# Performance work log

Measured on AMD Instinct MI355X. Metric: run time of the kernel, lower is better.

## Reference

```python
import jax, jax.numpy as jnp
import numpy as np

KS = 3  # kernel_size
PAD = 1  # padding


def setup_inputs() -> dict:
    key = jax.random.key(0)
    ks = jax.random.split(key, 5)
    b, c, h, w = 8, 64, 512, 512
    x = jax.random.normal(ks[0], (b, c, h, w), dtype=jnp.float32)
    w1 = jax.random.normal(ks[1], (c, c), dtype=jnp.float32) * 0.05
    b1 = jax.random.normal(ks[2], (c,), dtype=jnp.float32) * 0.05
    w2 = jax.random.normal(ks[3], (KS * KS, c), dtype=jnp.float32) * 0.05
    b2 = jax.random.normal(ks[4], (KS * KS,), dtype=jnp.float32) * 0.05
    return {"x": x, "w1": w1, "b1": b1, "w2": w2, "b2": b2}


def reference(x, w1, b1, w2, b2):
    b, c, h, w = x.shape
    # SEKG: global average pool -> 1x1 conv -> LeakyReLU(0.2) -> 1x1 conv
    feat = x.mean(axis=(2, 3))                      # [b, c]
    h1 = feat @ w1.T + b1                           # [b, c]
    h1 = jnp.where(h1 > 0, h1, 0.2 * h1)            # LeakyReLU(0.2)
    k = h1 @ w2.T + b2                              # [b, KS*KS]
    k = k.reshape(b, KS, KS)
    k = k / (k.sum(axis=(1, 2), keepdims=True) + 1e-6)  # normalize per-sample kernel
    # per-sample depthwise conv: fold batch into groups
    kern = jnp.broadcast_to(k[:, None], (b, c, KS, KS)).reshape(b * c, 1, KS, KS)
    xr = x.reshape(1, b * c, h, w)
    out = jax.lax.conv_general_dilated(
        xr, kern,
        window_strides=(1, 1),
        padding=[(PAD, PAD), (PAD, PAD)],
        feature_group_count=b * c,
        dimension_numbers=("NCHW", "OIHW", "NCHW"),
    )
    return out.reshape(b, c, h, w)
```

## Files before the change

kernel.cpp:

```cpp
#include <hip/hip_runtime.h>

#define HH 512
#define WW 512
#define HW (HH * WW)

typedef float f32x4 __attribute__((ext_vector_type(4)));

__device__ __forceinline__ void load_row6(float r[6], const float* __restrict__ plane,
                                          int y, int x0) {
    if ((unsigned)y >= (unsigned)HH) {
        r[0] = r[1] = r[2] = r[3] = r[4] = r[5] = 0.f;
        return;
    }
    const float* row = plane + (size_t)y * WW;
    r[0] = (x0 > 0) ? row[x0 - 1] : 0.f;
    const float4 m = *reinterpret_cast<const float4*>(row + x0);
    r[1] = m.x; r[2] = m.y; r[3] = m.z; r[4] = m.w;
    r[5] = (x0 + 4 < WW) ? row[x0 + 4] : 0.f;
}

__global__ __launch_bounds__(256) void stage_kernel(
        const float* __restrict__ x, float* __restrict__ out,
        float* __restrict__ partial,
        const float* __restrict__ w1, const float* __restrict__ b1,
        const float* __restrict__ w2, const float* __restrict__ b2,
        int ib, int nconv) {
    const int blk = blockIdx.x;
    const int t = threadIdx.x;

    if (blk < nconv) {
        const int b = ib - 1;
        __shared__ float feat[64];
        __shared__ float h1s[64];
        __shared__ float kks[10];
        if (t < 64) {
            const float* p4 = partial + (size_t)(b * 64 + t) * 4;
            feat[t] = (p4[0] + p4[1] + p4[2] + p4[3]) * (1.0f / (float)HW);
        }
        __syncthreads();
        if (t < 64) {
            float s = b1[t];
            const float* wr = w1 + t * 64;
            #pragma unroll 8
            for (int c = 0; c < 64; ++c) s += feat[c] * wr[c];
            h1s[t] = (s > 0.f) ? s : 0.2f * s;
        }
        __syncthreads();
        if (t < 9) {
            float s2 = b2[t];
            const float* wq = w2 + t * 64;
            #pragma unroll 8
            for (int c = 0; c < 64; ++c) s2 += h1s[c] * wq[c];
            kks[t] = s2;
        }
        __syncthreads();
        if (t == 0) {
            float s3 = 0.f;
            #pragma unroll
            for (int q = 0; q < 9; ++q) s3 += kks[q];
            kks[9] = s3 + 1e-6f;
        }
        __syncthreads();
        float k[9];
        {
            const float ks = kks[9];
            #pragma unroll
            for (int q = 0; q < 9; ++q) k[q] = kks[q] / ks;
        }

        const int plane_local = blk >> 4;
        const int plane = b * 64 + plane_local;
        const int xseg = t & 127;
        const int ystrip = ((blk & 15) << 1) | (t >> 7);
        const float* xp = x + (size_t)plane * HW;
        float* op       = out + (size_t)plane * HW;
        const int x0 = xseg * 4;
        const int y0 = ystrip * 16;

        float r0[6], r1[6], r2[6];
        load_row6(r0, xp, y0 - 1, x0);
        load_row6(r1, xp, y0,     x0);
        #pragma unroll
        for (int i = 0; i < 16; ++i) {
            load_row6(r2, xp, y0 + i + 1, x0);
            f32x4 o;
            #pragma unroll
            for (int j = 0; j < 4; ++j) {
                o[j] = k[0]*r0[j] + k[1]*r0[j+1] + k[2]*r0[j+2]
                     + k[3]*r1[j] + k[4]*r1[j+1] + k[5]*r1[j+2]
                     + k[6]*r2[j] + k[7]*r2[j+1] + k[8]*r2[j+2];
            }
            __builtin_nontemporal_store(o,
                reinterpret_cast<f32x4*>(op + (size_t)(y0 + i) * WW + x0));
            #pragma unroll
            for (int q = 0; q < 6; ++q) { r0[q] = r1[q]; r1[q] = r2[q]; }
        }
    } else {
        const int pblk = blk - nconv;
        const int plane = ib * 64 + (pblk >> 2);
        const int strip = pblk & 3;
        const float4* p = reinterpret_cast<const float4*>(x + (size_t)plane * HW) +
                          (size_t)strip * (HW / 16);
        float s = 0.f;
        #pragma unroll 4
        for (int i = t; i < HW / 16; i += 256) {
            float4 v = p[i];
            s += (v.x + v.y) + (v.z + v.w);
        }
        #pragma unroll
        for (int off = 32; off > 0; off >>= 1) s += __shfl_down(s, off, 64);
        __shared__ float wsum[4];
        const int lane = t & 63;
        const int wid  = t >> 6;
        if (lane == 0) wsum[wid] = s;
        __syncthreads();
        if (t == 0)
            partial[(size_t)plane * 4 + strip] =
                (wsum[0] + wsum[1]) + (wsum[2] + wsum[3]);
    }
}

extern "C" void kernel_launch(void* const* d_in, const int* in_sizes, int n_in,
                              void* d_out, int out_size, void* d_ws, size_t ws_size,
                              hipStream_t stream) {
    const float* x  = (const float*)d_in[0];
    const float* w1 = (const float*)d_in[1];
    const float* b1 = (const float*)d_in[2];
    const float* w2 = (const float*)d_in[3];
    const float* b2 = (const float*)d_in[4];
    float* out = (float*)d_out;
    float* partial = (float*)d_ws;

    stage_kernel<<<256, 256, 0, stream>>>(x, out, partial, w1, b1, w2, b2, 0, 0);
    for (int i = 1; i <= 7; ++i)
        stage_kernel<<<1280, 256, 0, stream>>>(x, out, partial, w1, b1, w2, b2, i, 1024);
    stage_kernel<<<1024, 256, 0, stream>>>(x, out, partial, w1, b1, w2, b2, 8, 1024);
}
```

Baseline: 302.2 us.

## Replace per-batch pipelined stages with a full pool pass and an XCD-mapped conv

The nine staggered launches, which overlapped pooling of batch i with convolution of batch i-1, are replaced by two kernels. One pass pools all planes, then a single conv grid runs over everything. Each conv block's batch is chosen from blockIdx & 7, so each XCD handles one batch's planes, which may improve L2 locality. In exchange the pool and conv phases no longer overlap, x is read twice without cache reuse between the stages, and every conv block recomputes the small MLP.

```diff
diff --git a/kernel.cpp b/kernel.cpp
--- a/kernel.cpp
+++ b/kernel.cpp
@@ -5,6 +5,29 @@
 #define HW (HH * WW)
 
 typedef float f32x4 __attribute__((ext_vector_type(4)));
+
+__global__ __launch_bounds__(256) void pool_kernel(const float* __restrict__ x,
+                                                   float* __restrict__ partial) {
+    const int blk = blockIdx.x;
+    const int plane = blk >> 2;
+    const int strip = blk & 3;
+    const float4* p = reinterpret_cast<const float4*>(x + (size_t)plane * HW) +
+                      (size_t)strip * (HW / 16);
+    float s = 0.f;
+    #pragma unroll 4
+    for (int i = threadIdx.x; i < HW / 16; i += 256) {
+        float4 v = p[i];
+        s += (v.x + v.y) + (v.z + v.w);
+    }
+    #pragma unroll
+    for (int off = 32; off > 0; off >>= 1) s += __shfl_down(s, off, 64);
+    __shared__ float wsum[4];
+    const int lane = threadIdx.x & 63;
+    const int wid  = threadIdx.x >> 6;
+    if (lane == 0) wsum[wid] = s;
+    __syncthreads();
+    if (threadIdx.x == 0) partial[blk] = (wsum[0] + wsum[1]) + (wsum[2] + wsum[3]);
+}
 
 __device__ __forceinline__ void load_row6(float r[6], const float* __restrict__ plane,
                                           int y, int x0) {
@@ -19,104 +42,84 @@
     r[5] = (x0 + 4 < WW) ? row[x0 + 4] : 0.f;
 }
 
-__global__ __launch_bounds__(256) void stage_kernel(
-        const float* __restrict__ x, float* __restrict__ out,
-        float* __restrict__ partial,
-        const float* __restrict__ w1, const float* __restrict__ b1,
-        const float* __restrict__ w2, const float* __restrict__ b2,
-        int ib, int nconv) {
-    const int blk = blockIdx.x;
-    const int t = threadIdx.x;
+__global__ __launch_bounds__(256) void conv_kernel(const float* __restrict__ x,
+                                                   const float* __restrict__ partial,
+                                                   const float* __restrict__ w1,
+                                                   const float* __restrict__ b1,
+                                                   const float* __restrict__ w2,
+                                                   const float* __restrict__ b2,
+                                                   float* __restrict__ out) {
+    const int bid = blockIdx.x;
+    const int t   = threadIdx.x;
+    const int xcd = bid & 7;
+    const int j   = bid >> 3;
+    const int b   = xcd;
 
-    if (blk < nconv) {
-        const int b = ib - 1;
-        __shared__ float feat[64];
-        __shared__ float h1s[64];
-        __shared__ float kks[10];
-        if (t < 64) {
-            const float* p4 = partial + (size_t)(b * 64 + t) * 4;
-            feat[t] = (p4[0] + p4[1] + p4[2] + p4[3]) * (1.0f / (float)HW);
+    __shared__ float feat[64];
+    __shared__ float h1s[64];
+    __shared__ float kks[10];
+    if (t < 64) {
+        const float* p4 = partial + (size_t)(b * 64 + t) * 4;
+        feat[t] = (p4[0] + p4[1] + p4[2] + p4[3]) * (1.0f / (float)HW);
+    }
+    __syncthreads();
+    if (t < 64) {
+        float s = b1[t];
+        const float* wr = w1 + t * 64;
+        #pragma unroll 8
+        for (int c = 0; c < 64; ++c) s += feat[c] * wr[c];
+        h1s[t] = (s > 0.f) ? s : 0.2f * s;
+    }
+    __syncthreads();
+    if (t < 9) {
+        float s2 = b2[t];
+        const float* wq = w2 + t * 64;
+        #pragma unroll 8
+        for (int c = 0; c < 64; ++c) s2 += h1s[c] * wq[c];
+        kks[t] = s2;
+    }
+    __syncthreads();
+    if (t == 0) {
+        float s3 = 0.f;
+        #pragma unroll
+        for (int q = 0; q < 9; ++q) s3 += kks[q];
+        kks[9] = s3 + 1e-6f;
+    }
+    __syncthreads();
+    float k[9];
+    {
+        const float ks = kks[9];
+        #pragma unroll
+        for (int q = 0; q < 9; ++q) k[q] = kks[q] / ks;
+    }
+
+    const int plane_local = j >> 4;
+    const int band        = j & 15;
+    const int plane = xcd * 64 + plane_local;
+    const int xseg = t & 127;
+    const int ystrip = (band << 1) | (t >> 7);
+    const float* xp = x + (size_t)plane * HW;
+    float* op       = out + (size_t)plane * HW;
+    const int x0 = xseg * 4;
+    const int y0 = ystrip * 16;
+
+    float r0[6], r1[6], r2[6];
+    load_row6(r0, xp, y0 - 1, x0);
+    load_row6(r1, xp, y0,     x0);
+    #pragma unroll
+    for (int i = 0; i < 16; ++i) {
+        load_row6(r2, xp, y0 + i + 1, x0);
+        f32x4 o;
+        #pragma unroll
+        for (int jj = 0; jj < 4; ++jj) {
+            o[jj] = k[0]*r0[jj] + k[1]*r0[jj+1] + k[2]*r0[jj+2]
+                  + k[3]*r1[jj] + k[4]*r1[jj+1] + k[5]*r1[jj+2]
+                  + k[6]*r2[jj] + k[7]*r2[jj+1] + k[8]*r2[jj+2];
         }
-        __syncthreads();
-        if (t < 64) {
-            float s = b1[t];
-            const float* wr = w1 + t * 64;
-            #pragma unroll 8
-            for (int c = 0; c < 64; ++c) s += feat[c] * wr[c];
-            h1s[t] = (s > 0.f) ? s : 0.2f * s;
-        }
-        __syncthreads();
-        if (t < 9) {
-            float s2 = b2[t];
-            const float* wq = w2 + t * 64;
-            #pragma unroll 8
-            for (int c = 0; c < 64; ++c) s2 += h1s[c] * wq[c];
-            kks[t] = s2;
-        }
-        __syncthreads();
-        if (t == 0) {
-            float s3 = 0.f;
-            #pragma unroll
-            for (int q = 0; q < 9; ++q) s3 += kks[q];
-            kks[9] = s3 + 1e-6f;
-        }
-        __syncthreads();
-        float k[9];
-        {
-            const float ks = kks[9];
-            #pragma unroll
-            for (int q = 0; q < 9; ++q) k[q] = kks[q] / ks;
-        }
-
-        const int plane_local = blk >> 4;
-        const int plane = b * 64 + plane_local;
-        const int xseg = t & 127;
-        const int ystrip = ((blk & 15) << 1) | (t >> 7);
-        const float* xp = x + (size_t)plane * HW;
-        float* op       = out + (size_t)plane * HW;
-        const int x0 = xseg * 4;
-        const int y0 = ystrip * 16;
-
-        float r0[6], r1[6], r2[6];
-        load_row6(r0, xp, y0 - 1, x0);
-        load_row6(r1, xp, y0,     x0);
+        __builtin_nontemporal_store(o,
+            reinterpret_cast<f32x4*>(op + (size_t)(y0 + i) * WW + x0));
         #pragma unroll
-        for (int i = 0; i < 16; ++i) {
-            load_row6(r2, xp, y0 + i + 1, x0);
-            f32x4 o;
-            #pragma unroll
-            for (int j = 0; j < 4; ++j) {
-                o[j] = k[0]*r0[j] + k[1]*r0[j+1] + k[2]*r0[j+2]
-                     + k[3]*r1[j] + k[4]*r1[j+1] + k[5]*r1[j+2]
-                     + k[6]*r2[j] + k[7]*r2[j+1] + k[8]*r2[j+2];
-            }
-            __builtin_nontemporal_store(o,
-                reinterpret_cast<f32x4*>(op + (size_t)(y0 + i) * WW + x0));
-            #pragma unroll
-            for (int q = 0; q < 6; ++q) { r0[q] = r1[q]; r1[q] = r2[q]; }
-        }
-    } else {
-        const int pblk = blk - nconv;
-        const int plane = ib * 64 + (pblk >> 2);
-        const int strip = pblk & 3;
-        const float4* p = reinterpret_cast<const float4*>(x + (size_t)plane * HW) +
-                          (size_t)strip * (HW / 16);
-        float s = 0.f;
-        #pragma unroll 4
-        for (int i = t; i < HW / 16; i += 256) {
-            float4 v = p[i];
-            s += (v.x + v.y) + (v.z + v.w);
-        }
-        #pragma unroll
-        for (int off = 32; off > 0; off >>= 1) s += __shfl_down(s, off, 64);
-        __shared__ float wsum[4];
-        const int lane = t & 63;
-        const int wid  = t >> 6;
-        if (lane == 0) wsum[wid] = s;
-        __syncthreads();
-        if (t == 0)
-            partial[(size_t)plane * 4 + strip] =
-                (wsum[0] + wsum[1]) + (wsum[2] + wsum[3]);
+        for (int q = 0; q < 6; ++q) { r0[q] = r1[q]; r1[q] = r2[q]; }
     }
 }
 
@@ -131,8 +134,6 @@
     float* out = (float*)d_out;
     float* partial = (float*)d_ws;
 
-    stage_kernel<<<256, 256, 0, stream>>>(x, out, partial, w1, b1, w2, b2, 0, 0);
-    for (int i = 1; i <= 7; ++i)
-        stage_kernel<<<1280, 256, 0, stream>>>(x, out, partial, w1, b1, w2, b2, i, 1024);
-    stage_kernel<<<1024, 256, 0, stream>>>(x, out, partial, w1, b1, w2, b2, 8, 1024);
+    pool_kernel<<<2048, 256, 0, stream>>>(x, partial);
+    conv_kernel<<<8192, 256, 0, stream>>>(x, partial, w1, b1, w2, b2, out);
 }
```

Result: slower. 309.7 us (+2.5%).
